# Kernel optimization log

Hardware: AMD Instinct MI355X
Metric: run time of the kernel (lower is better)

Reference implementation:

```python
import jax, jax.numpy as jnp
import numpy as np

N_NODES = 50000
N_EDGES = 800000
N_RELS = 65
D = 64
N_GRAPHS = 512


def setup_inputs() -> dict:
    key = jax.random.key(0)
    ks = jax.random.split(key, 20)
    inp = {
        "node_feats": jax.random.normal(ks[0], (N_NODES, D), dtype=jnp.float32),
        "etypes": jax.random.randint(ks[1], (N_EDGES,), 0, N_RELS),
        "src": jax.random.randint(ks[2], (N_EDGES,), 0, N_NODES),
        "dst": jax.random.randint(ks[3], (N_EDGES,), 0, N_NODES),
        "graph_ids": jnp.sort(jax.random.randint(ks[4], (N_NODES,), 0, N_GRAPHS)),
    }
    s = 1.0 / np.sqrt(D)
    # 3 RGCN layers: per-relation weights (basis with num_bases=num_rels == full) + bias
    for i, k in zip(range(1, 4), (ks[5], ks[6], ks[7])):
        inp[f"W_rel{i}"] = jax.random.normal(k, (N_RELS, D, D), dtype=jnp.float32) * s
        inp[f"b{i}"] = jnp.zeros((D,), dtype=jnp.float32)
    # 3 FC layers
    for i, k in zip(range(1, 4), (ks[8], ks[9], ks[10])):
        inp[f"fc_W{i}"] = jax.random.normal(k, (D, D), dtype=jnp.float32) * s
        inp[f"fc_b{i}"] = jnp.zeros((D,), dtype=jnp.float32)
    inp["pred_W"] = jax.random.normal(ks[11], (D, 2), dtype=jnp.float32) * s
    inp["pred_b"] = jnp.zeros((2,), dtype=jnp.float32)
    return inp


def _rgcn_layer(h, W, b, etypes, src, dst):
    # all-relation projection: [N, R, K]
    proj = jnp.einsum('nd,rdk->nrk', h, W)
    # per-edge gather of relation-specific message: [E, K]
    msg = proj[src, etypes]
    # scatter-sum into destination nodes
    agg = jax.ops.segment_sum(msg, dst, num_segments=h.shape[0])
    return jax.nn.relu(agg + b)


def reference(node_feats, etypes, src, dst, graph_ids,
              W_rel1, b1, W_rel2, b2, W_rel3, b3,
              fc_W1, fc_b1, fc_W2, fc_b2, fc_W3, fc_b3,
              pred_W, pred_b):
    h = node_feats
    h = _rgcn_layer(h, W_rel1, b1, etypes, src, dst)
    h = _rgcn_layer(h, W_rel2, b2, etypes, src, dst)
    h = _rgcn_layer(h, W_rel3, b3, etypes, src, dst)
    # sum-pool nodes per graph: [G, D]
    g = jax.ops.segment_sum(h, graph_ids, num_segments=N_GRAPHS)
    g = jax.nn.relu(g @ fc_W1 + fc_b1)
    g = jax.nn.relu(g @ fc_W2 + fc_b2)
    g = jax.nn.relu(g @ fc_W3 + fc_b3)
    return g @ pred_W + pred_b
```

## Files before the change

### kernel.cpp

```cpp
#include <hip/hip_runtime.h>
#include <hip/hip_bf16.h>

#define N_NODES 50000
#define N_EDGES 800000
#define N_RELS 65
#define DIM 64
#define N_GRAPHS 512

#define SORT_BLOCKS 1024
#define CHUNK ((N_EDGES + SORT_BLOCKS - 1) / SORT_BLOCKS)

#define SCAN_BLK 512
#define NSCAN_BLKS ((N_NODES + SCAN_BLK - 1) / SCAN_BLK)

#define MSG_BLOCKS 1024
#define NWAVES (MSG_BLOCKS * 4)

typedef __attribute__((ext_vector_type(8))) short short8;
typedef __attribute__((ext_vector_type(4))) float f32x4;


__global__ void conv_h_zero_kernel(const float* __restrict__ x, __hip_bfloat16* __restrict__ y,
                                   int* __restrict__ cnt_d, int* __restrict__ cnt_g) {
    int i = blockIdx.x * 256 + threadIdx.x;
    if (i < (N_NODES * DIM) / 4) {
        float4 v = *(const float4*)(x + (size_t)i * 4);
        unsigned short us[4];
        us[0] = __hip_bfloat16_raw(__float2bfloat16(v.x)).x;
        us[1] = __hip_bfloat16_raw(__float2bfloat16(v.y)).x;
        us[2] = __hip_bfloat16_raw(__float2bfloat16(v.z)).x;
        us[3] = __hip_bfloat16_raw(__float2bfloat16(v.w)).x;
        *(ushort4*)(y + (size_t)i * 4) = *(const ushort4*)us;
    }
    if (i < N_NODES) cnt_d[i] = 0;
    if (i < N_GRAPHS) cnt_g[i] = 0;
}


__global__ __launch_bounds__(256) void hist_all_kernel(
    const int* __restrict__ et, const int* __restrict__ gid,
    int* __restrict__ blk_hist, int* __restrict__ cnt_g,
    const float* __restrict__ W1, const float* __restrict__ W2,
    const float* __restrict__ W3,
    __hip_bfloat16* __restrict__ Wt1, __hip_bfloat16* __restrict__ Wt2,
    __hip_bfloat16* __restrict__ Wt3) {
    __shared__ int lh[N_RELS];
    int t = threadIdx.x, b = blockIdx.x;
    int gtid = b * 256 + t;
    if (t < N_RELS) lh[t] = 0;
    __syncthreads();
    int lo = b * CHUNK;
    int hi = lo + CHUNK; if (hi > N_EDGES) hi = N_EDGES;
    for (int i = lo + t; i < hi; i += 256)
        atomicAdd(&lh[et[i]], 1);
    for (int i = gtid; i < N_NODES; i += SORT_BLOCKS * 256)
        atomicAdd(&cnt_g[gid[i]], 1);
    const int WN = N_RELS * DIM * DIM;
    for (int i = gtid; i < 3 * WN; i += SORT_BLOCKS * 256) {
        int which = i / WN, j = i - which * WN;
        const float* W = (which == 0) ? W1 : (which == 1) ? W2 : W3;
        __hip_bfloat16* Wt = (which == 0) ? Wt1 : (which == 1) ? Wt2 : Wt3;
        int r = j >> 12, rest = j & 4095;
        int nn = rest >> 6, k = rest & 63;
        Wt[(size_t)r * 4096 + nn * 64 + k] =
            __float2bfloat16(W[(size_t)r * 4096 + k * 64 + nn]);
    }
    __syncthreads();
    if (t < N_RELS) blk_hist[t * SORT_BLOCKS + b] = lh[t];
}


__global__ __launch_bounds__(1024) void relwave2_kernel(const int* __restrict__ blk_hist,
                                                        int* __restrict__ blk_off,
                                                        int* __restrict__ rel_ptr,
                                                        int* __restrict__ tile_base) {
    __shared__ int tot[N_RELS];
    int t = threadIdx.x;
    int w = t >> 6, lane = t & 63;
    for (int r = w; r < N_RELS; r += 16) {
        int run = 0;
        for (int c = 0; c < SORT_BLOCKS; c += 64) {
            int b = c + lane;
            int v = blk_hist[r * SORT_BLOCKS + b];
            int x = v;
            #pragma unroll
            for (int off = 1; off < 64; off <<= 1) {
                int y = __shfl_up(x, off);
                if (lane >= off) x += y;
            }
            blk_off[r * SORT_BLOCKS + b] = run + x - v;
            run += __shfl(x, 63);
        }
        if (lane == 0) tot[r] = run;
    }
    __syncthreads();
    if (t == 0) {
        int s = 0, tt = 0;
        for (int q = 0; q < N_RELS; ++q) {
            rel_ptr[q] = s; s += tot[q];
            tile_base[q] = tt; tt += (tot[q] + 15) >> 4;
        }
        rel_ptr[N_RELS] = N_EDGES;
        tile_base[N_RELS] = tt;
    }
}


__global__ __launch_bounds__(256) void scatter2_kernel(
    const int* __restrict__ et, const int* __restrict__ src,
    const int* __restrict__ dst, const int* __restrict__ blk_off,
    const int* __restrict__ rel_ptr,
    unsigned long long* __restrict__ epk, int* __restrict__ cnt_d) {
    __shared__ int cur[N_RELS];
    int t = threadIdx.x, b = blockIdx.x;
    if (t < N_RELS) cur[t] = blk_off[t * SORT_BLOCKS + b] + rel_ptr[t];
    __syncthreads();
    int lo = b * CHUNK;
    int hi = lo + CHUNK; if (hi > N_EDGES) hi = N_EDGES;

    bool val[4]; int rr[4], dd[4]; unsigned ss[4];
    #pragma unroll
    for (int k = 0; k < 4; ++k) {
        int i = lo + t + k * 256;
        val[k] = (i < hi);
        int ic = val[k] ? i : lo;
        rr[k] = et[ic]; dd[k] = dst[ic]; ss[k] = (unsigned)src[ic];
    }
    int p[4];
    #pragma unroll
    for (int k = 0; k < 4; ++k)
        if (val[k]) p[k] = atomicAdd(&cur[rr[k]], 1);
    int rk[4];
    #pragma unroll
    for (int k = 0; k < 4; ++k)
        if (val[k]) rk[k] = atomicAdd(&cnt_d[dd[k]], 1);
    #pragma unroll
    for (int k = 0; k < 4; ++k)
        if (val[k]) {
            unsigned lo32 = ss[k] | ((unsigned)dd[k] << 16);
            epk[p[k]] = (unsigned long long)lo32 |
                        ((unsigned long long)(unsigned)rk[k] << 32);
        }
}


__global__ __launch_bounds__(SCAN_BLK) void scanblk_kernel(const int* __restrict__ cnt,
                                                           int* __restrict__ outv,
                                                           int* __restrict__ blk_tot) {
    __shared__ int tmp[SCAN_BLK];
    int t = threadIdx.x;
    int i = blockIdx.x * SCAN_BLK + t;
    int v = (i < N_NODES) ? cnt[i] : 0;
    tmp[t] = v;
    __syncthreads();
    for (int off = 1; off < SCAN_BLK; off <<= 1) {
        int add = (t >= off) ? tmp[t - off] : 0;
        __syncthreads();
        tmp[t] += add;
        __syncthreads();
    }
    if (i < N_NODES) outv[i] = tmp[t] - v;
    if (t == SCAN_BLK - 1) blk_tot[blockIdx.x] = tmp[t];
}

__global__ __launch_bounds__(64) void scantop_gid_kernel(
    const int* __restrict__ blk_tot, int* __restrict__ blk_base,
    const int* __restrict__ cnt_g, int* __restrict__ g_ptr) {
    int lane = threadIdx.x;
    if (blockIdx.x == 0) {
        if (lane == 0) {
            int run = 0;
            for (int b = 0; b < NSCAN_BLKS; ++b) { blk_base[b] = run; run += blk_tot[b]; }
        }
    } else {
        int run = 0;
        for (int c = 0; c < N_GRAPHS; c += 64) {
            int v = cnt_g[c + lane];
            int x = v;
            #pragma unroll
            for (int off = 1; off < 64; off <<= 1) {
                int y = __shfl_up(x, off);
                if (lane >= off) x += y;
            }
            g_ptr[c + lane] = run + x - v;
            run += __shfl(x, 63);
        }
    }
}

__global__ __launch_bounds__(SCAN_BLK) void scanadd_kernel(int* __restrict__ outv,
                                                           const int* __restrict__ blk_base) {
    int i = blockIdx.x * SCAN_BLK + threadIdx.x;
    if (i < N_NODES) outv[i] += blk_base[blockIdx.x];
}

__global__ void unpack_kernel(const unsigned long long* __restrict__ epk,
                              const int* __restrict__ row_ptr,
                              int* __restrict__ src_s, int* __restrict__ dpos) {
    int i = blockIdx.x * 256 + threadIdx.x;
    if (i < N_EDGES) {
        unsigned long long e = epk[i];
        int s = (int)(e & 0xFFFFu);
        int d = (int)((e >> 16) & 0xFFFFu);
        int rank = (int)(e >> 32);
        src_s[i] = s;
        dpos[i] = rank + row_ptr[d];
    }
}


__global__ __launch_bounds__(256) void msg_mfma_kernel(
    const __hip_bfloat16* __restrict__ hb, const __hip_bfloat16* __restrict__ Wt,
    const int* __restrict__ rel_ptr, const int* __restrict__ tile_base,
    const int* __restrict__ src_s, const int* __restrict__ dpos,
    __hip_bfloat16* __restrict__ msg) {
    __shared__ __align__(16) unsigned short stA[4][16 * 72];
    __shared__ __align__(16) float stC[4][16 * 68];

    int t = threadIdx.x;
    int w = t >> 6, lane = t & 63;
    int quad = lane >> 4, m16 = lane & 15;
    int wave = blockIdx.x * 4 + w;

    int ntiles = tile_base[N_RELS];
    int tpw = (ntiles + NWAVES - 1) / NWAVES;
    int T = wave * tpw;
    int T1 = T + tpw; if (T1 > ntiles) T1 = ntiles;
    if (T >= T1) return;

    unsigned short* sa = &stA[w][0];
    float* sc = &stC[w][0];
    int r0l = lane >> 3;

    int r = 0;
    while (T >= tile_base[r + 1]) ++r;

    while (T < T1) {
        int chunk_end = tile_base[r + 1]; if (chunk_end > T1) chunk_end = T1;
        int e_base = rel_ptr[r], t_base = tile_base[r];
        int seg_end = rel_ptr[r + 1];

        const __hip_bfloat16* Wr = Wt + (size_t)r * (DIM * DIM);
        short8 bf00 = *(const short8*)(Wr + (0 * 16 + m16) * DIM + quad * 8);
        short8 bf01 = *(const short8*)(Wr + (1 * 16 + m16) * DIM + quad * 8);
        short8 bf02 = *(const short8*)(Wr + (2 * 16 + m16) * DIM + quad * 8);
        short8 bf03 = *(const short8*)(Wr + (3 * 16 + m16) * DIM + quad * 8);
        short8 bf10 = *(const short8*)(Wr + (0 * 16 + m16) * DIM + 32 + quad * 8);
        short8 bf11 = *(const short8*)(Wr + (1 * 16 + m16) * DIM + 32 + quad * 8);
        short8 bf12 = *(const short8*)(Wr + (2 * 16 + m16) * DIM + 32 + quad * 8);
        short8 bf13 = *(const short8*)(Wr + (3 * 16 + m16) * DIM + 32 + quad * 8);

        auto loadidx = [&](int TT, int& sv, int& dp) {
            int TC = TT < chunk_end ? TT : chunk_end - 1;
            int i = e_base + (TC - t_base) * 16 + lane;
            if (i >= N_EDGES) i = N_EDGES - 1;
            sv = src_s[i]; dp = dpos[i];
        };
        auto gather = [&](int sv, uint4& g0, uint4& g1) {
            int s0 = __shfl(sv, r0l);
            int s1 = __shfl(sv, r0l + 8);
            g0 = *(const uint4*)(hb + (size_t)s0 * DIM + (lane & 7) * 8);
            g1 = *(const uint4*)(hb + (size_t)s1 * DIM + (lane & 7) * 8);
        };

        int sv0, dp0, sv1, dp1, sv2, dp2, sv3, dp3;
        uint4 gc0, gc1, gn0, gn1;
        loadidx(T,     sv0, dp0);
        loadidx(T + 1, sv1, dp1);
        loadidx(T + 2, sv2, dp2);
        gather(sv0, gc0, gc1);
        gather(sv1, gn0, gn1);

        for (; T < chunk_end; ++T) {
            int e0 = e_base + (T - t_base) * 16;
            int rows = seg_end - e0; if (rows > 16) rows = 16;

            uint4 gnn0, gnn1;
            gather(sv2, gnn0, gnn1);
            loadidx(T + 3, sv3, dp3);

            *(uint4*)&sa[r0l * 72 + (lane & 7) * 8] = gc0;
            *(uint4*)&sa[(r0l + 8) * 72 + (lane & 7) * 8] = gc1;

            short8 a0 = *(const short8*)&sa[m16 * 72 + quad * 8];
            short8 a1 = *(const short8*)&sa[m16 * 72 + 32 + quad * 8];

            f32x4 c0 = {0.f, 0.f, 0.f, 0.f}, c1 = c0, c2 = c0, c3 = c0;
            c0 = __builtin_amdgcn_mfma_f32_16x16x32_bf16(a0, bf00, c0, 0, 0, 0);
            c1 = __builtin_amdgcn_mfma_f32_16x16x32_bf16(a0, bf01, c1, 0, 0, 0);
            c2 = __builtin_amdgcn_mfma_f32_16x16x32_bf16(a0, bf02, c2, 0, 0, 0);
            c3 = __builtin_amdgcn_mfma_f32_16x16x32_bf16(a0, bf03, c3, 0, 0, 0);
            c0 = __builtin_amdgcn_mfma_f32_16x16x32_bf16(a1, bf10, c0, 0, 0, 0);
            c1 = __builtin_amdgcn_mfma_f32_16x16x32_bf16(a1, bf11, c1, 0, 0, 0);
            c2 = __builtin_amdgcn_mfma_f32_16x16x32_bf16(a1, bf12, c2, 0, 0, 0);
            c3 = __builtin_amdgcn_mfma_f32_16x16x32_bf16(a1, bf13, c3, 0, 0, 0);

            #pragma unroll
            for (int reg = 0; reg < 4; ++reg) {
                int rr2 = (quad * 4 + reg) * 68 + m16;
                sc[rr2 +  0] = c0[reg];
                sc[rr2 + 16] = c1[reg];
                sc[rr2 + 32] = c2[reg];
                sc[rr2 + 48] = c3[reg];
            }

            int orow = lane >> 2;
            if (orow < rows) {
                int c0i = (lane & 3) * 16;
                float vs[16];
                *(f32x4*)&vs[0]  = *(const f32x4*)&sc[orow * 68 + c0i + 0];
                *(f32x4*)&vs[4]  = *(const f32x4*)&sc[orow * 68 + c0i + 4];
                *(f32x4*)&vs[8]  = *(const f32x4*)&sc[orow * 68 + c0i + 8];
                *(f32x4*)&vs[12] = *(const f32x4*)&sc[orow * 68 + c0i + 12];
                unsigned short us[16];
                #pragma unroll
                for (int i = 0; i < 16; ++i)
                    us[i] = __hip_bfloat16_raw(__float2bfloat16(vs[i])).x;
                int dprow = __shfl(dp0, orow);
                __hip_bfloat16* dstp = msg + (size_t)dprow * DIM + c0i;
                *(uint4*)dstp = *(const uint4*)&us[0];
                *(uint4*)(dstp + 8) = *(const uint4*)&us[8];
            }

            gc0 = gn0; gc1 = gn1; gn0 = gnn0; gn1 = gnn1;
            sv0 = sv1; dp0 = dp1; sv1 = sv2; dp1 = dp2; sv2 = sv3; dp2 = dp3;
        }
        ++r;
        while (T < T1 && T >= tile_base[r + 1]) ++r;
    }
}


__global__ __launch_bounds__(256) void agg_kernel(
    const __hip_bfloat16* __restrict__ msg, const int* __restrict__ row_ptr,
    const int* __restrict__ cnt_d, const float* __restrict__ b,
    __hip_bfloat16* __restrict__ hout) {
    int wave = blockIdx.x * 4 + (threadIdx.x >> 6);
    int lane = threadIdx.x & 63;
    if (wave >= N_NODES) return;
    int j0 = row_ptr[wave];
    int n  = cnt_d[wave];
    int rgrp = lane >> 3, dgrp = lane & 7;

    float a[8] = {0.f, 0.f, 0.f, 0.f, 0.f, 0.f, 0.f, 0.f};
    for (int jj = 0; jj < n; jj += 8) {
        int row = jj + rgrp;
        if (row < n) {
            uint4 d = *(const uint4*)(msg + (size_t)(j0 + row) * DIM + dgrp * 8);
            a[0] += __uint_as_float(d.x << 16);
            a[1] += __uint_as_float(d.x & 0xffff0000u);
            a[2] += __uint_as_float(d.y << 16);
            a[3] += __uint_as_float(d.y & 0xffff0000u);
            a[4] += __uint_as_float(d.z << 16);
            a[5] += __uint_as_float(d.z & 0xffff0000u);
            a[6] += __uint_as_float(d.w << 16);
            a[7] += __uint_as_float(d.w & 0xffff0000u);
        }
    }
    #pragma unroll
    for (int i = 0; i < 8; ++i) {
        a[i] += __shfl_xor(a[i], 8);
        a[i] += __shfl_xor(a[i], 16);
        a[i] += __shfl_xor(a[i], 32);
    }
    if (rgrp == 0) {
        unsigned short us[8];
        #pragma unroll
        for (int i = 0; i < 8; ++i) {
            float v = a[i] + b[dgrp * 8 + i];
            us[i] = __hip_bfloat16_raw(__float2bfloat16(v > 0.f ? v : 0.f)).x;
        }
        *(uint4*)(hout + (size_t)wave * DIM + dgrp * 8) = *(const uint4*)us;
    }
}


__global__ __launch_bounds__(256) void poolfc_kernel(
    const __hip_bfloat16* __restrict__ h, const int* __restrict__ g_ptr,
    const int* __restrict__ cnt_g,
    const float* __restrict__ W1, const float* __restrict__ b1,
    const float* __restrict__ W2, const float* __restrict__ b2,
    const float* __restrict__ W3, const float* __restrict__ b3,
    const float* __restrict__ pW, const float* __restrict__ pb,
    float* __restrict__ out) {
    int wave = blockIdx.x * 4 + (threadIdx.x >> 6);
    int lane = threadIdx.x & 63;
    if (wave >= N_GRAPHS) return;
    int j0 = g_ptr[wave];
    int n  = cnt_g[wave];
    int rgrp = lane >> 3, dgrp = lane & 7;

    float a[8] = {0.f, 0.f, 0.f, 0.f, 0.f, 0.f, 0.f, 0.f};
    for (int jj = 0; jj < n; jj += 8) {
        int row = jj + rgrp;
        if (row < n) {
            uint4 d = *(const uint4*)(h + (size_t)(j0 + row) * DIM + dgrp * 8);
            a[0] += __uint_as_float(d.x << 16);
            a[1] += __uint_as_float(d.x & 0xffff0000u);
            a[2] += __uint_as_float(d.y << 16);
            a[3] += __uint_as_float(d.y & 0xffff0000u);
            a[4] += __uint_as_float(d.z << 16);
            a[5] += __uint_as_float(d.z & 0xffff0000u);
            a[6] += __uint_as_float(d.w << 16);
            a[7] += __uint_as_float(d.w & 0xffff0000u);
        }
    }
    #pragma unroll
    for (int i = 0; i < 8; ++i) {
        a[i] += __shfl_xor(a[i], 8);
        a[i] += __shfl_xor(a[i], 16);
        a[i] += __shfl_xor(a[i], 32);
    }
    float v;
    {
        float acc = b1[lane];
        #pragma unroll
        for (int o = 0; o < 8; ++o)
            #pragma unroll
            for (int q = 0; q < 8; ++q)
                acc += __shfl(a[o], q) * W1[(q * 8 + o) * DIM + lane];
        v = acc > 0.f ? acc : 0.f;
    }
    {
        float acc = b2[lane];
        #pragma unroll
        for (int d = 0; d < DIM; ++d)
            acc += __shfl(v, d) * W2[d * DIM + lane];
        v = acc > 0.f ? acc : 0.f;
    }
    {
        float acc = b3[lane];
        #pragma unroll
        for (int d = 0; d < DIM; ++d)
            acc += __shfl(v, d) * W3[d * DIM + lane];
        v = acc > 0.f ? acc : 0.f;
    }
    float p0 = v * pW[lane * 2 + 0];
    float p1 = v * pW[lane * 2 + 1];
    #pragma unroll
    for (int off = 32; off > 0; off >>= 1) {
        p0 += __shfl_down(p0, off);
        p1 += __shfl_down(p1, off);
    }
    if (lane == 0) {
        out[wave * 2 + 0] = p0 + pb[0];
        out[wave * 2 + 1] = p1 + pb[1];
    }
}


extern "C" void kernel_launch(void* const* d_in, const int* in_sizes, int n_in,
                              void* d_out, int out_size, void* d_ws, size_t ws_size,
                              hipStream_t stream) {
    const float* node_feats = (const float*)d_in[0];
    const int*   etypes     = (const int*)d_in[1];
    const int*   src        = (const int*)d_in[2];
    const int*   dst        = (const int*)d_in[3];
    const int*   graph_ids  = (const int*)d_in[4];
    const float* W1 = (const float*)d_in[5];
    const float* b1 = (const float*)d_in[6];
    const float* W2 = (const float*)d_in[7];
    const float* b2 = (const float*)d_in[8];
    const float* W3 = (const float*)d_in[9];
    const float* b3 = (const float*)d_in[10];
    const float* fcW1 = (const float*)d_in[11];
    const float* fcb1 = (const float*)d_in[12];
    const float* fcW2 = (const float*)d_in[13];
    const float* fcb2 = (const float*)d_in[14];
    const float* fcW3 = (const float*)d_in[15];
    const float* fcb3 = (const float*)d_in[16];
    const float* pW = (const float*)d_in[17];
    const float* pb = (const float*)d_in[18];
    float* out = (float*)d_out;

    char* p = (char*)d_ws;
    auto alloc = [&](size_t bytes) -> void* {
        void* r = (void*)p;
        p += (bytes + 255) & ~(size_t)255;
        return r;
    };
    int* blk_hist  = (int*)alloc((size_t)SORT_BLOCKS * N_RELS * sizeof(int));
    int* blk_off   = (int*)alloc((size_t)SORT_BLOCKS * N_RELS * sizeof(int));
    int* rel_ptr   = (int*)alloc((N_RELS + 1) * sizeof(int));
    int* tile_base = (int*)alloc((N_RELS + 1) * sizeof(int));
    unsigned long long* epk = (unsigned long long*)alloc((size_t)N_EDGES * sizeof(unsigned long long));
    int* src_s     = (int*)alloc((size_t)N_EDGES * sizeof(int));
    int* dpos      = (int*)alloc((size_t)N_EDGES * sizeof(int));
    int* cnt_d     = (int*)alloc((size_t)N_NODES * sizeof(int));
    int* row_ptr   = (int*)alloc((size_t)N_NODES * sizeof(int));
    int* blk_tot   = (int*)alloc(NSCAN_BLKS * sizeof(int));
    int* blk_base  = (int*)alloc(NSCAN_BLKS * sizeof(int));
    int* cnt_g     = (int*)alloc(N_GRAPHS * sizeof(int));
    int* g_ptr     = (int*)alloc(N_GRAPHS * sizeof(int));
    __hip_bfloat16* hb0 = (__hip_bfloat16*)alloc((size_t)N_NODES * DIM * sizeof(__hip_bfloat16));
    __hip_bfloat16* hb1 = (__hip_bfloat16*)alloc((size_t)N_NODES * DIM * sizeof(__hip_bfloat16));
    __hip_bfloat16* Wt1 = (__hip_bfloat16*)alloc((size_t)N_RELS * DIM * DIM * sizeof(__hip_bfloat16));
    __hip_bfloat16* Wt2 = (__hip_bfloat16*)alloc((size_t)N_RELS * DIM * DIM * sizeof(__hip_bfloat16));
    __hip_bfloat16* Wt3 = (__hip_bfloat16*)alloc((size_t)N_RELS * DIM * DIM * sizeof(__hip_bfloat16));
    __hip_bfloat16* msg = (__hip_bfloat16*)alloc((size_t)N_EDGES * DIM * sizeof(__hip_bfloat16));

    const int EBLK = (N_EDGES + 255) / 256;
    const int CBLK = (N_NODES * DIM / 4 + 255) / 256;
    const int AGG_BLOCKS = (N_NODES + 3) / 4;

    conv_h_zero_kernel<<<CBLK, 256, 0, stream>>>(node_feats, hb0, cnt_d, cnt_g);
    hist_all_kernel<<<SORT_BLOCKS, 256, 0, stream>>>(etypes, graph_ids, blk_hist, cnt_g,
                                                     W1, W2, W3, Wt1, Wt2, Wt3);
    relwave2_kernel<<<1, 1024, 0, stream>>>(blk_hist, blk_off, rel_ptr, tile_base);
    scatter2_kernel<<<SORT_BLOCKS, 256, 0, stream>>>(etypes, src, dst, blk_off, rel_ptr,
                                                     epk, cnt_d);
    scanblk_kernel<<<NSCAN_BLKS, SCAN_BLK, 0, stream>>>(cnt_d, row_ptr, blk_tot);
    scantop_gid_kernel<<<2, 64, 0, stream>>>(blk_tot, blk_base, cnt_g, g_ptr);
    scanadd_kernel<<<NSCAN_BLKS, SCAN_BLK, 0, stream>>>(row_ptr, blk_base);
    unpack_kernel<<<EBLK, 256, 0, stream>>>(epk, row_ptr, src_s, dpos);

    msg_mfma_kernel<<<MSG_BLOCKS, 256, 0, stream>>>(hb0, Wt1, rel_ptr, tile_base,
                                                    src_s, dpos, msg);
    agg_kernel<<<AGG_BLOCKS, 256, 0, stream>>>(msg, row_ptr, cnt_d, b1, hb1);

    msg_mfma_kernel<<<MSG_BLOCKS, 256, 0, stream>>>(hb1, Wt2, rel_ptr, tile_base,
                                                    src_s, dpos, msg);
    agg_kernel<<<AGG_BLOCKS, 256, 0, stream>>>(msg, row_ptr, cnt_d, b2, hb0);

    msg_mfma_kernel<<<MSG_BLOCKS, 256, 0, stream>>>(hb0, Wt3, rel_ptr, tile_base,
                                                    src_s, dpos, msg);
    agg_kernel<<<AGG_BLOCKS, 256, 0, stream>>>(msg, row_ptr, cnt_d, b3, hb1);

    poolfc_kernel<<<(N_GRAPHS + 3) / 4, 256, 0, stream>>>(hb1, g_ptr, cnt_g,
                                                          fcW1, fcb1, fcW2, fcb2,
                                                          fcW3, fcb3, pW, pb, out);
}
```

Baseline: 389.5 us.

## Gather MFMA operands directly to registers and drop LDS staging in message kernel

```diff
diff --git a/kernel.cpp b/kernel.cpp
--- a/kernel.cpp
+++ b/kernel.cpp
@@ -7,13 +7,13 @@
 #define DIM 64
 #define N_GRAPHS 512
 
-#define SORT_BLOCKS 1024
+#define SORT_BLOCKS 2048
 #define CHUNK ((N_EDGES + SORT_BLOCKS - 1) / SORT_BLOCKS)
 
 #define SCAN_BLK 512
 #define NSCAN_BLKS ((N_NODES + SCAN_BLK - 1) / SCAN_BLK)
 
-#define MSG_BLOCKS 1024
+#define MSG_BLOCKS 2048
 #define NWAVES (MSG_BLOCKS * 4)
 
 typedef __attribute__((ext_vector_type(8))) short short8;
@@ -37,13 +37,32 @@
 }
 
 
-__global__ __launch_bounds__(256) void hist_all_kernel(
-    const int* __restrict__ et, const int* __restrict__ gid,
-    int* __restrict__ blk_hist, int* __restrict__ cnt_g,
+__global__ __launch_bounds__(256) void wconv_kernel(
     const float* __restrict__ W1, const float* __restrict__ W2,
     const float* __restrict__ W3,
     __hip_bfloat16* __restrict__ Wt1, __hip_bfloat16* __restrict__ Wt2,
     __hip_bfloat16* __restrict__ Wt3) {
+    __shared__ float tile[64][65];
+    int b = blockIdx.x;
+    int which = b / N_RELS, r = b - which * N_RELS;
+    const float* W = (which == 0) ? W1 : (which == 1) ? W2 : W3;
+    __hip_bfloat16* Wt = (which == 0) ? Wt1 : (which == 1) ? Wt2 : Wt3;
+    int t = threadIdx.x;
+    for (int i = t; i < 4096; i += 256) {
+        int row = i >> 6, col = i & 63;
+        tile[row][col] = W[(size_t)r * 4096 + i];
+    }
+    __syncthreads();
+    for (int i = t; i < 4096; i += 256) {
+        int row = i >> 6, col = i & 63;
+        Wt[(size_t)r * 4096 + i] = __float2bfloat16(tile[col][row]);
+    }
+}
+
+
+__global__ __launch_bounds__(256) void hist_all_kernel(
+    const int* __restrict__ et, const int* __restrict__ gid,
+    int* __restrict__ blk_hist, int* __restrict__ cnt_g) {
     __shared__ int lh[N_RELS];
     int t = threadIdx.x, b = blockIdx.x;
     int gtid = b * 256 + t;
@@ -55,16 +74,6 @@
         atomicAdd(&lh[et[i]], 1);
     for (int i = gtid; i < N_NODES; i += SORT_BLOCKS * 256)
         atomicAdd(&cnt_g[gid[i]], 1);
-    const int WN = N_RELS * DIM * DIM;
-    for (int i = gtid; i < 3 * WN; i += SORT_BLOCKS * 256) {
-        int which = i / WN, j = i - which * WN;
-        const float* W = (which == 0) ? W1 : (which == 1) ? W2 : W3;
-        __hip_bfloat16* Wt = (which == 0) ? Wt1 : (which == 1) ? Wt2 : Wt3;
-        int r = j >> 12, rest = j & 4095;
-        int nn = rest >> 6, k = rest & 63;
-        Wt[(size_t)r * 4096 + nn * 64 + k] =
-            __float2bfloat16(W[(size_t)r * 4096 + k * 64 + nn]);
-    }
     __syncthreads();
     if (t < N_RELS) blk_hist[t * SORT_BLOCKS + b] = lh[t];
 }
@@ -209,14 +218,17 @@
 }
 
 
+__device__ inline unsigned pack2bf(float x, float y) {
+    unsigned short ux = __hip_bfloat16_raw(__float2bfloat16(x)).x;
+    unsigned short uy = __hip_bfloat16_raw(__float2bfloat16(y)).x;
+    return (unsigned)ux | ((unsigned)uy << 16);
+}
+
 __global__ __launch_bounds__(256) void msg_mfma_kernel(
     const __hip_bfloat16* __restrict__ hb, const __hip_bfloat16* __restrict__ Wt,
     const int* __restrict__ rel_ptr, const int* __restrict__ tile_base,
     const int* __restrict__ src_s, const int* __restrict__ dpos,
     __hip_bfloat16* __restrict__ msg) {
-    __shared__ __align__(16) unsigned short stA[4][16 * 72];
-    __shared__ __align__(16) float stC[4][16 * 68];
-
     int t = threadIdx.x;
     int w = t >> 6, lane = t & 63;
     int quad = lane >> 4, m16 = lane & 15;
@@ -228,10 +240,6 @@
     int T1 = T + tpw; if (T1 > ntiles) T1 = ntiles;
     if (T >= T1) return;
 
-    unsigned short* sa = &stA[w][0];
-    float* sc = &stC[w][0];
-    int r0l = lane >> 3;
-
     int r = 0;
     while (T >= tile_base[r + 1]) ++r;
 
@@ -241,14 +249,14 @@
         int seg_end = rel_ptr[r + 1];
 
         const __hip_bfloat16* Wr = Wt + (size_t)r * (DIM * DIM);
-        short8 bf00 = *(const short8*)(Wr + (0 * 16 + m16) * DIM + quad * 8);
-        short8 bf01 = *(const short8*)(Wr + (1 * 16 + m16) * DIM + quad * 8);
-        short8 bf02 = *(const short8*)(Wr + (2 * 16 + m16) * DIM + quad * 8);
-        short8 bf03 = *(const short8*)(Wr + (3 * 16 + m16) * DIM + quad * 8);
-        short8 bf10 = *(const short8*)(Wr + (0 * 16 + m16) * DIM + 32 + quad * 8);
-        short8 bf11 = *(const short8*)(Wr + (1 * 16 + m16) * DIM + 32 + quad * 8);
-        short8 bf12 = *(const short8*)(Wr + (2 * 16 + m16) * DIM + 32 + quad * 8);
-        short8 bf13 = *(const short8*)(Wr + (3 * 16 + m16) * DIM + 32 + quad * 8);
+        short8 bf00 = *(const short8*)(Wr + (2 * m16)      * DIM + quad * 8);
+        short8 bf01 = *(const short8*)(Wr + (2 * m16 + 1)  * DIM + quad * 8);
+        short8 bf02 = *(const short8*)(Wr + (32 + 2 * m16) * DIM + quad * 8);
+        short8 bf03 = *(const short8*)(Wr + (33 + 2 * m16) * DIM + quad * 8);
+        short8 bf10 = *(const short8*)(Wr + (2 * m16)      * DIM + 32 + quad * 8);
+        short8 bf11 = *(const short8*)(Wr + (2 * m16 + 1)  * DIM + 32 + quad * 8);
+        short8 bf12 = *(const short8*)(Wr + (32 + 2 * m16) * DIM + 32 + quad * 8);
+        short8 bf13 = *(const short8*)(Wr + (33 + 2 * m16) * DIM + 32 + quad * 8);
 
         auto loadidx = [&](int TT, int& sv, int& dp) {
             int TC = TT < chunk_end ? TT : chunk_end - 1;
@@ -256,74 +264,53 @@
             if (i >= N_EDGES) i = N_EDGES - 1;
             sv = src_s[i]; dp = dpos[i];
         };
-        auto gather = [&](int sv, uint4& g0, uint4& g1) {
-            int s0 = __shfl(sv, r0l);
-            int s1 = __shfl(sv, r0l + 8);
-            g0 = *(const uint4*)(hb + (size_t)s0 * DIM + (lane & 7) * 8);
-            g1 = *(const uint4*)(hb + (size_t)s1 * DIM + (lane & 7) * 8);
+        auto gatherA = [&](int sv, short8& x0, short8& x1) {
+            int s = __shfl(sv, m16);
+            const __hip_bfloat16* hp = hb + (size_t)s * DIM + quad * 8;
+            x0 = *(const short8*)hp;
+            x1 = *(const short8*)(hp + 32);
         };
 
-        int sv0, dp0, sv1, dp1, sv2, dp2, sv3, dp3;
-        uint4 gc0, gc1, gn0, gn1;
+        int sv0, dp0, sv1, dp1, sv2, dp2;
+        short8 a0c, a1c, a0n, a1n;
         loadidx(T,     sv0, dp0);
         loadidx(T + 1, sv1, dp1);
-        loadidx(T + 2, sv2, dp2);
-        gather(sv0, gc0, gc1);
-        gather(sv1, gn0, gn1);
+        gatherA(sv0, a0c, a1c);
 
         for (; T < chunk_end; ++T) {
+            loadidx(T + 2, sv2, dp2);
+            gatherA(sv1, a0n, a1n);
+
             int e0 = e_base + (T - t_base) * 16;
             int rows = seg_end - e0; if (rows > 16) rows = 16;
 
-            uint4 gnn0, gnn1;
-            gather(sv2, gnn0, gnn1);
-            loadidx(T + 3, sv3, dp3);
-
-            *(uint4*)&sa[r0l * 72 + (lane & 7) * 8] = gc0;
-            *(uint4*)&sa[(r0l + 8) * 72 + (lane & 7) * 8] = gc1;
-
-            short8 a0 = *(const short8*)&sa[m16 * 72 + quad * 8];
-            short8 a1 = *(const short8*)&sa[m16 * 72 + 32 + quad * 8];
-
             f32x4 c0 = {0.f, 0.f, 0.f, 0.f}, c1 = c0, c2 = c0, c3 = c0;
-            c0 = __builtin_amdgcn_mfma_f32_16x16x32_bf16(a0, bf00, c0, 0, 0, 0);
-            c1 = __builtin_amdgcn_mfma_f32_16x16x32_bf16(a0, bf01, c1, 0, 0, 0);
-            c2 = __builtin_amdgcn_mfma_f32_16x16x32_bf16(a0, bf02, c2, 0, 0, 0);
-            c3 = __builtin_amdgcn_mfma_f32_16x16x32_bf16(a0, bf03, c3, 0, 0, 0);
-            c0 = __builtin_amdgcn_mfma_f32_16x16x32_bf16(a1, bf10, c0, 0, 0, 0);
-            c1 = __builtin_amdgcn_mfma_f32_16x16x32_bf16(a1, bf11, c1, 0, 0, 0);
-            c2 = __builtin_amdgcn_mfma_f32_16x16x32_bf16(a1, bf12, c2, 0, 0, 0);
-            c3 = __builtin_amdgcn_mfma_f32_16x16x32_bf16(a1, bf13, c3, 0, 0, 0);
-
+            c0 = __builtin_amdgcn_mfma_f32_16x16x32_bf16(a0c, bf00, c0, 0, 0, 0);
+            c1 = __builtin_amdgcn_mfma_f32_16x16x32_bf16(a0c, bf01, c1, 0, 0, 0);
+            c2 = __builtin_amdgcn_mfma_f32_16x16x32_bf16(a0c, bf02, c2, 0, 0, 0);
+            c3 = __builtin_amdgcn_mfma_f32_16x16x32_bf16(a0c, bf03, c3, 0, 0, 0);
+            c0 = __builtin_amdgcn_mfma_f32_16x16x32_bf16(a1c, bf10, c0, 0, 0, 0);
+            c1 = __builtin_amdgcn_mfma_f32_16x16x32_bf16(a1c, bf11, c1, 0, 0, 0);
+            c2 = __builtin_amdgcn_mfma_f32_16x16x32_bf16(a1c, bf12, c2, 0, 0, 0);
+            c3 = __builtin_amdgcn_mfma_f32_16x16x32_bf16(a1c, bf13, c3, 0, 0, 0);
+
+            int dpr[4];
             #pragma unroll
-            for (int reg = 0; reg < 4; ++reg) {
-                int rr2 = (quad * 4 + reg) * 68 + m16;
-                sc[rr2 +  0] = c0[reg];
-                sc[rr2 + 16] = c1[reg];
-                sc[rr2 + 32] = c2[reg];
-                sc[rr2 + 48] = c3[reg];
+            for (int g = 0; g < 4; ++g) dpr[g] = __shfl(dp0, quad * 4 + g);
+
+            #pragma unroll
+            for (int g = 0; g < 4; ++g) {
+                if (quad * 4 + g < rows) {
+                    unsigned plo = pack2bf(c0[g], c1[g]);
+                    unsigned phi = pack2bf(c2[g], c3[g]);
+                    __hip_bfloat16* mp = msg + (size_t)dpr[g] * DIM;
+                    *(unsigned*)(mp + 2 * m16) = plo;
+                    *(unsigned*)(mp + 32 + 2 * m16) = phi;
+                }
             }
 
-            int orow = lane >> 2;
-            if (orow < rows) {
-                int c0i = (lane & 3) * 16;
-                float vs[16];
-                *(f32x4*)&vs[0]  = *(const f32x4*)&sc[orow * 68 + c0i + 0];
-                *(f32x4*)&vs[4]  = *(const f32x4*)&sc[orow * 68 + c0i + 4];
-                *(f32x4*)&vs[8]  = *(const f32x4*)&sc[orow * 68 + c0i + 8];
-                *(f32x4*)&vs[12] = *(const f32x4*)&sc[orow * 68 + c0i + 12];
-                unsigned short us[16];
-                #pragma unroll
-                for (int i = 0; i < 16; ++i)
-                    us[i] = __hip_bfloat16_raw(__float2bfloat16(vs[i])).x;
-                int dprow = __shfl(dp0, orow);
-                __hip_bfloat16* dstp = msg + (size_t)dprow * DIM + c0i;
-                *(uint4*)dstp = *(const uint4*)&us[0];
-                *(uint4*)(dstp + 8) = *(const uint4*)&us[8];
-            }
-
-            gc0 = gn0; gc1 = gn1; gn0 = gnn0; gn1 = gnn1;
-            sv0 = sv1; dp0 = dp1; sv1 = sv2; dp1 = dp2; sv2 = sv3; dp2 = dp3;
+            sv0 = sv1; dp0 = dp1; sv1 = sv2; dp1 = dp2;
+            a0c = a0n; a1c = a1n;
         }
         ++r;
         while (T < T1 && T >= tile_base[r + 1]) ++r;
@@ -504,8 +491,8 @@
     const int AGG_BLOCKS = (N_NODES + 3) / 4;
 
     conv_h_zero_kernel<<<CBLK, 256, 0, stream>>>(node_feats, hb0, cnt_d, cnt_g);
-    hist_all_kernel<<<SORT_BLOCKS, 256, 0, stream>>>(etypes, graph_ids, blk_hist, cnt_g,
-                                                     W1, W2, W3, Wt1, Wt2, Wt3);
+    wconv_kernel<<<3 * N_RELS, 256, 0, stream>>>(W1, W2, W3, Wt1, Wt2, Wt3);
+    hist_all_kernel<<<SORT_BLOCKS, 256, 0, stream>>>(etypes, graph_ids, blk_hist, cnt_g);
     relwave2_kernel<<<1, 1024, 0, stream>>>(blk_hist, blk_off, rel_ptr, tile_base);
     scatter2_kernel<<<SORT_BLOCKS, 256, 0, stream>>>(etypes, src, dst, blk_off, rel_ptr,
                                                      epk, cnt_d);
```

Result: slower. 420.5 us (+7.9%).
